# Optimization experiments

Measured on AMD Instinct MI355X. Metric: run time of the kernel, lower is better.

Reference implementation:

```python
import jax, jax.numpy as jnp
import numpy as np

NUM_TOPICS = 64
VOCAB_SIZE = 50000
BATCH = 2048
RHO = 0.1

def setup_inputs() -> dict:
    key = jax.random.key(0)
    k_x, k_b, k_t, k_m = jax.random.split(key, 4)
    x = jax.random.uniform(k_x, (BATCH, VOCAB_SIZE), dtype=jnp.float32)  # BoW-like counts
    beta = jax.random.normal(k_b, (NUM_TOPICS, VOCAB_SIZE), dtype=jnp.float32)
    theta = jax.random.normal(k_t, (NUM_TOPICS, NUM_TOPICS), dtype=jnp.float32)
    mu = jax.random.normal(k_m, (NUM_TOPICS,), dtype=jnp.float32)
    return {"x": x, "beta": beta, "theta": theta, "mu": mu}

def reference(x, beta, theta, mu):
    # Original double loop:
    #   log_prob[:,k] = sum(x*beta[k],1) + mu[k] + rho * sum_{j!=k} theta[k,j]*sum(x*beta[j],1)
    # Let s[b,k] = sum_v x[b,v]*beta[k,v] = (x @ beta.T)[b,k].
    # Then log_prob = s + mu + rho * s @ (theta with zeroed diagonal).T
    s = jnp.einsum('bv,kv->bk', x, beta)                      # [B, K]
    theta_off = theta * (1.0 - jnp.eye(theta.shape[0], dtype=theta.dtype))
    log_prob = s + mu[None, :] + RHO * jnp.einsum('bj,kj->bk', s, theta_off)
    return log_prob
```

## Files before the change

kernel.cpp:

```cpp
#include <hip/hip_runtime.h>

typedef unsigned short u16;
typedef unsigned int u32;
typedef unsigned long long u64;

#define VOCAB 50000
#define BATCH 2048
#define NTOP 64
#define RHO 0.1f

#define KSPLIT 32
#define CHUNK 1568
#define KSTEP 64

typedef short bf16x4 __attribute__((ext_vector_type(4)));
typedef short bf16x8 __attribute__((ext_vector_type(8)));
typedef float f32x4 __attribute__((ext_vector_type(4)));

__device__ __forceinline__ u32 cvtpk(float lo, float hi) {
  u32 r;
  asm volatile("v_cvt_pk_bf16_f32 %0, %1, %2" : "=v"(r) : "v"(lo), "v"(hi));
  return r;
}
union frag_cast { bf16x4 h[2]; bf16x8 v; };

__global__ void __launch_bounds__(256, 4) ctm_gemm(const float* __restrict__ x,
                                                   const float* __restrict__ beta,
                                                   float* __restrict__ sp) {
  __shared__ u16 ldsA[2][64 * KSTEP];
  __shared__ u16 ldsB[2][64 * KSTEP];

  const int t = threadIdx.x;
  const int l = t & 63;
  const int w = t >> 6;
  const int fr = l & 15;
  const int fk = l >> 4;

  const int bx = blockIdx.x;
  const int k0 = bx * CHUNK;
  const int kend = (k0 + CHUNK < VOCAB) ? (k0 + CHUNK) : VOCAB;
  const int row0 = blockIdx.y * 64;
  const int nsteps = (kend - k0 + KSTEP - 1) >> 6;

  const int c = t & 15;
  const int srow = t >> 4;
  const float* xb = x + (u64)(row0 + srow) * VOCAB + k0 + c * 4;
  const float* betab = beta + (u64)srow * VOCAB + k0 + c * 4;
  const u32 wofs = (u32)(srow * 128) + (((u32)(c * 8)) ^ ((u32)((srow & 7) << 4)));

  const int arow = w * 16 + fr;
  const u32 arb = (u32)(arow * 128);
  const u32 aswz = (u32)((arow & 7) << 4);

  f32x4 acc[4] = {{0.f,0.f,0.f,0.f},{0.f,0.f,0.f,0.f},{0.f,0.f,0.f,0.f},{0.f,0.f,0.f,0.f}};

  {
    const int rem = kend - k0 < KSTEP ? kend - k0 : KSTEP;
    const bool m = (c * 4) < rem;
    float4 a0 = make_float4(0,0,0,0), a1 = a0, a2 = a0, a3 = a0;
    float4 b0 = a0, b1 = a0, b2 = a0, b3 = a0;
    if (m) {
      a0 = *(const float4*)(xb);               b0 = *(const float4*)(betab);
      a1 = *(const float4*)(xb + 16 * VOCAB);  b1 = *(const float4*)(betab + 16 * VOCAB);
      a2 = *(const float4*)(xb + 32 * VOCAB);  b2 = *(const float4*)(betab + 32 * VOCAB);
      a3 = *(const float4*)(xb + 48 * VOCAB);  b3 = *(const float4*)(betab + 48 * VOCAB);
    }
    *(uint2*)((char*)ldsA[0] + wofs)        = make_uint2(cvtpk(a0.x,a0.y), cvtpk(a0.z,a0.w));
    *(uint2*)((char*)ldsA[0] + wofs + 2048) = make_uint2(cvtpk(a1.x,a1.y), cvtpk(a1.z,a1.w));
    *(uint2*)((char*)ldsA[0] + wofs + 4096) = make_uint2(cvtpk(a2.x,a2.y), cvtpk(a2.z,a2.w));
    *(uint2*)((char*)ldsA[0] + wofs + 6144) = make_uint2(cvtpk(a3.x,a3.y), cvtpk(a3.z,a3.w));
    *(uint2*)((char*)ldsB[0] + wofs)        = make_uint2(cvtpk(b0.x,b0.y), cvtpk(b0.z,b0.w));
    *(uint2*)((char*)ldsB[0] + wofs + 2048) = make_uint2(cvtpk(b1.x,b1.y), cvtpk(b1.z,b1.w));
    *(uint2*)((char*)ldsB[0] + wofs + 4096) = make_uint2(cvtpk(b2.x,b2.y), cvtpk(b2.z,b2.w));
    *(uint2*)((char*)ldsB[0] + wofs + 6144) = make_uint2(cvtpk(b3.x,b3.y), cvtpk(b3.z,b3.w));
  }
  __syncthreads();

  for (int st = 0; st < nsteps; ++st) {
    const int cb = st & 1;
    const bool have_next = (st + 1) < nsteps;

    float4 a0, a1, a2, a3, b0, b1, b2, b3;
    if (have_next) {
      const int ks = (st + 1) << 6;
      const int rem = kend - k0 - ks;
      const bool m = (c * 4) < rem;
      a0 = a1 = a2 = a3 = make_float4(0,0,0,0);
      b0 = b1 = b2 = b3 = make_float4(0,0,0,0);
      if (m) {
        const float* xp = xb + ks;
        const float* bp2 = betab + ks;
        a0 = *(const float4*)(xp);               b0 = *(const float4*)(bp2);
        a1 = *(const float4*)(xp + 16 * VOCAB);  b1 = *(const float4*)(bp2 + 16 * VOCAB);
        a2 = *(const float4*)(xp + 32 * VOCAB);  b2 = *(const float4*)(bp2 + 32 * VOCAB);
        a3 = *(const float4*)(xp + 48 * VOCAB);  b3 = *(const float4*)(bp2 + 48 * VOCAB);
      }
    }

    const char* bufA = (const char*)ldsA[cb];
    const char* bufB = (const char*)ldsB[cb];
    #pragma unroll
    for (int s = 0; s < 2; ++s) {
      const u32 in0 = (u32)(s * 64 + fk * 8);
      const u32 in1 = in0 + 32;
      frag_cast ua;
      ua.h[0] = *(const bf16x4*)(bufA + arb + (in0 ^ aswz));
      ua.h[1] = *(const bf16x4*)(bufA + arb + (in1 ^ aswz));
      #pragma unroll
      for (int n = 0; n < 4; ++n) {
        const int bcol = (n << 4) | fr;
        const u32 brb = (u32)(bcol * 128);
        const u32 bswz = (u32)((bcol & 7) << 4);
        frag_cast ub;
        ub.h[0] = *(const bf16x4*)(bufB + brb + (in0 ^ bswz));
        ub.h[1] = *(const bf16x4*)(bufB + brb + (in1 ^ bswz));
        acc[n] = __builtin_amdgcn_mfma_f32_16x16x32_bf16(ua.v, ub.v, acc[n], 0, 0, 0);
      }
    }

    if (have_next) {
      char* nA = (char*)ldsA[cb ^ 1];
      char* nB = (char*)ldsB[cb ^ 1];
      *(uint2*)(nA + wofs)        = make_uint2(cvtpk(a0.x,a0.y), cvtpk(a0.z,a0.w));
      *(uint2*)(nA + wofs + 2048) = make_uint2(cvtpk(a1.x,a1.y), cvtpk(a1.z,a1.w));
      *(uint2*)(nA + wofs + 4096) = make_uint2(cvtpk(a2.x,a2.y), cvtpk(a2.z,a2.w));
      *(uint2*)(nA + wofs + 6144) = make_uint2(cvtpk(a3.x,a3.y), cvtpk(a3.z,a3.w));
      *(uint2*)(nB + wofs)        = make_uint2(cvtpk(b0.x,b0.y), cvtpk(b0.z,b0.w));
      *(uint2*)(nB + wofs + 2048) = make_uint2(cvtpk(b1.x,b1.y), cvtpk(b1.z,b1.w));
      *(uint2*)(nB + wofs + 4096) = make_uint2(cvtpk(b2.x,b2.y), cvtpk(b2.z,b2.w));
      *(uint2*)(nB + wofs + 6144) = make_uint2(cvtpk(b3.x,b3.y), cvtpk(b3.z,b3.w));
      __syncthreads();
    }
  }

  float* spb = sp + (u64)bx * (BATCH * NTOP);
  const int orow = row0 + w * 16 + fk * 4;
  #pragma unroll
  for (int n = 0; n < 4; ++n) {
    #pragma unroll
    for (int r = 0; r < 4; ++r)
      spb[(orow + r) * NTOP + ((n << 4) | fr)] = acc[n][r];
  }
}

__global__ void __launch_bounds__(256) ctm_epi(const float* __restrict__ sp,
                                               const float* __restrict__ theta,
                                               const float* __restrict__ mu,
                                               float* __restrict__ out) {
  __shared__ float thT[NTOP * NTOP];
  __shared__ float sb[8 * NTOP];
  const int t = threadIdx.x;
  const int r0 = blockIdx.x * 8;

  #pragma unroll
  for (int i = 0; i < 16; ++i) {
    int e = i * 256 + t;
    thT[(e & 63) * 64 + (e >> 6)] = theta[e];
  }

  const int k = t & 63;
  const int rl = t >> 6;
  #pragma unroll
  for (int rr = 0; rr < 2; ++rr) {
    const int r = rl + rr * 4;
    float sum = 0.f;
    #pragma unroll
    for (int cc = 0; cc < KSPLIT; ++cc)
      sum += sp[(u64)cc * (BATCH * NTOP) + (r0 + r) * NTOP + k];
    sb[r * 64 + k] = sum;
  }
  __syncthreads();

  const float muk = mu[k];
  const float diag = thT[k * 64 + k];
  #pragma unroll
  for (int rr = 0; rr < 2; ++rr) {
    const int r = rl + rr * 4;
    const float* srow = &sb[r * 64];
    float accv = 0.f;
    #pragma unroll 8
    for (int j = 0; j < 64; ++j)
      accv += thT[j * 64 + k] * srow[j];
    const float sv = srow[k];
    out[(r0 + r) * 64 + k] = sv + muk + RHO * (accv - diag * sv);
  }
}

extern "C" void kernel_launch(void* const* d_in, const int* in_sizes, int n_in,
                              void* d_out, int out_size, void* d_ws, size_t ws_size,
                              hipStream_t stream) {
  const float* x = (const float*)d_in[0];
  const float* beta = (const float*)d_in[1];
  const float* theta = (const float*)d_in[2];
  const float* mu = (const float*)d_in[3];
  float* out = (float*)d_out;

  float* sp = (float*)d_ws;

  ctm_gemm<<<dim3(KSPLIT, BATCH / 64), 256, 0, stream>>>(x, beta, sp);
  ctm_epi<<<BATCH / 8, 256, 0, stream>>>(sp, theta, mu, out);
}
```

Measured before the change: 109.7 us.

## Use direct global-to-LDS loads with triple buffering and half-precision partials

Result: no change. 111.3 us (+1.5%).

```diff
diff --git a/kernel.cpp b/kernel.cpp
--- a/kernel.cpp
+++ b/kernel.cpp
@@ -1,4 +1,5 @@
 #include <hip/hip_runtime.h>
+#include <hip/hip_fp16.h>
 
 typedef unsigned short u16;
 typedef unsigned int u32;
@@ -9,9 +10,10 @@
 #define NTOP 64
 #define RHO 0.1f
 
-#define KSPLIT 32
-#define CHUNK 1568
-#define KSTEP 64
+#define KSPLIT 24
+#define CHUNK 2112
+#define KSTEP 32
+#define BUFB 16384
 
 typedef short bf16x4 __attribute__((ext_vector_type(4)));
 typedef short bf16x8 __attribute__((ext_vector_type(8)));
@@ -22,13 +24,12 @@
   asm volatile("v_cvt_pk_bf16_f32 %0, %1, %2" : "=v"(r) : "v"(lo), "v"(hi));
   return r;
 }
-union frag_cast { bf16x4 h[2]; bf16x8 v; };
-
-__global__ void __launch_bounds__(256, 4) ctm_gemm(const float* __restrict__ x,
+union frag_cast { u32 w[4]; bf16x8 v; };
+
+__global__ void __launch_bounds__(256, 3) ctm_gemm(const float* __restrict__ x,
                                                    const float* __restrict__ beta,
-                                                   float* __restrict__ sp) {
-  __shared__ u16 ldsA[2][64 * KSTEP];
-  __shared__ u16 ldsB[2][64 * KSTEP];
+                                                   __half* __restrict__ sp) {
+  __shared__ u16 lds[3 * BUFB / 2];
 
   const int t = threadIdx.x;
   const int l = t & 63;
@@ -40,110 +41,129 @@
   const int k0 = bx * CHUNK;
   const int kend = (k0 + CHUNK < VOCAB) ? (k0 + CHUNK) : VOCAB;
   const int row0 = blockIdx.y * 64;
-  const int nsteps = (kend - k0 + KSTEP - 1) >> 6;
-
-  const int c = t & 15;
-  const int srow = t >> 4;
-  const float* xb = x + (u64)(row0 + srow) * VOCAB + k0 + c * 4;
-  const float* betab = beta + (u64)srow * VOCAB + k0 + c * 4;
-  const u32 wofs = (u32)(srow * 128) + (((u32)(c * 8)) ^ ((u32)((srow & 7) << 4)));
+  const int nfull = (kend - k0) >> 5;
+  const int rem = (kend - k0) & 31;
+
+  const int sr = t >> 3;
+  const int so = t & 7;
+  const int swf = 4 * (so ^ (sr & 7));
+  const float* xs0 = x + (u64)(row0 + sr) * VOCAB + k0 + swf;
+  const float* xs1 = xs0 + (u64)32 * VOCAB;
+  const float* bs0 = beta + (u64)sr * VOCAB + k0 + swf;
+  const float* bs1 = bs0 + (u64)32 * VOCAB;
+  const u32 dA0 = (u32)(t * 16), dA1 = dA0 + 4096;
+  const u32 dB0 = dA0 + 8192,   dB1 = dA0 + 12288;
 
   const int arow = w * 16 + fr;
   const u32 arb = (u32)(arow * 128);
   const u32 aswz = (u32)((arow & 7) << 4);
+  const u32 aof0 = (u32)(fk * 16) ^ aswz;
+  const u32 aof1 = (u32)(64 + fk * 16) ^ aswz;
 
   f32x4 acc[4] = {{0.f,0.f,0.f,0.f},{0.f,0.f,0.f,0.f},{0.f,0.f,0.f,0.f},{0.f,0.f,0.f,0.f}};
 
-  {
-    const int rem = kend - k0 < KSTEP ? kend - k0 : KSTEP;
-    const bool m = (c * 4) < rem;
-    float4 a0 = make_float4(0,0,0,0), a1 = a0, a2 = a0, a3 = a0;
-    float4 b0 = a0, b1 = a0, b2 = a0, b3 = a0;
-    if (m) {
-      a0 = *(const float4*)(xb);               b0 = *(const float4*)(betab);
-      a1 = *(const float4*)(xb + 16 * VOCAB);  b1 = *(const float4*)(betab + 16 * VOCAB);
-      a2 = *(const float4*)(xb + 32 * VOCAB);  b2 = *(const float4*)(betab + 32 * VOCAB);
-      a3 = *(const float4*)(xb + 48 * VOCAB);  b3 = *(const float4*)(betab + 48 * VOCAB);
+#define STAGE(slot, st)                                                          \
+  {                                                                              \
+    const u32 b_ = (u32)(slot) * BUFB;                                           \
+    const u64 ko_ = (u64)((st) * KSTEP);                                         \
+    __builtin_amdgcn_global_load_lds(                                            \
+        (const __attribute__((address_space(1))) void*)(xs0 + ko_),              \
+        (__attribute__((address_space(3))) void*)((char*)lds + b_ + dA0), 16, 0, 0); \
+    __builtin_amdgcn_global_load_lds(                                            \
+        (const __attribute__((address_space(1))) void*)(xs1 + ko_),              \
+        (__attribute__((address_space(3))) void*)((char*)lds + b_ + dA1), 16, 0, 0); \
+    __builtin_amdgcn_global_load_lds(                                            \
+        (const __attribute__((address_space(1))) void*)(bs0 + ko_),              \
+        (__attribute__((address_space(3))) void*)((char*)lds + b_ + dB0), 16, 0, 0); \
+    __builtin_amdgcn_global_load_lds(                                            \
+        (const __attribute__((address_space(1))) void*)(bs1 + ko_),              \
+        (__attribute__((address_space(3))) void*)((char*)lds + b_ + dB1), 16, 0, 0); \
+  }
+
+#define COMPUTE(slot)                                                            \
+  {                                                                              \
+    const char* bufA = (const char*)lds + (u32)(slot) * BUFB;                    \
+    const char* bufB = bufA + 8192;                                              \
+    f32x4 q0 = *(const f32x4*)(bufA + arb + aof0);                               \
+    f32x4 q1 = *(const f32x4*)(bufA + arb + aof1);                               \
+    frag_cast ua;                                                                \
+    ua.w[0] = cvtpk(q0.x, q0.y); ua.w[1] = cvtpk(q0.z, q0.w);                    \
+    ua.w[2] = cvtpk(q1.x, q1.y); ua.w[3] = cvtpk(q1.z, q1.w);                    \
+    _Pragma("unroll")                                                            \
+    for (int n = 0; n < 4; ++n) {                                                \
+      const int bcol = n * 16 + fr;                                              \
+      const u32 brb = (u32)(bcol * 128);                                         \
+      const u32 bswz = (u32)((bcol & 7) << 4);                                   \
+      f32x4 p0 = *(const f32x4*)(bufB + brb + (((u32)(fk * 16)) ^ bswz));        \
+      f32x4 p1 = *(const f32x4*)(bufB + brb + (((u32)(64 + fk * 16)) ^ bswz));   \
+      frag_cast ub;                                                              \
+      ub.w[0] = cvtpk(p0.x, p0.y); ub.w[1] = cvtpk(p0.z, p0.w);                  \
+      ub.w[2] = cvtpk(p1.x, p1.y); ub.w[3] = cvtpk(p1.z, p1.w);                  \
+      acc[n] = __builtin_amdgcn_mfma_f32_16x16x32_bf16(ua.v, ub.v, acc[n], 0, 0, 0); \
+    }                                                                            \
+  }
+
+  STAGE(0, 0);
+  STAGE(1, 1);
+
+  int slot = 0;
+  for (int st = 0; st < nfull; ++st) {
+    if (st + 1 < nfull) asm volatile("s_waitcnt vmcnt(4)" ::: "memory");
+    else                asm volatile("s_waitcnt vmcnt(0)" ::: "memory");
+    __builtin_amdgcn_s_barrier();
+    __builtin_amdgcn_sched_barrier(0);
+    if (st + 2 < nfull) {
+      const int ns = (slot + 2 >= 3) ? (slot - 1) : (slot + 2);
+      STAGE(ns, st + 2);
     }
-    *(uint2*)((char*)ldsA[0] + wofs)        = make_uint2(cvtpk(a0.x,a0.y), cvtpk(a0.z,a0.w));
-    *(uint2*)((char*)ldsA[0] + wofs + 2048) = make_uint2(cvtpk(a1.x,a1.y), cvtpk(a1.z,a1.w));
-    *(uint2*)((char*)ldsA[0] + wofs + 4096) = make_uint2(cvtpk(a2.x,a2.y), cvtpk(a2.z,a2.w));
-    *(uint2*)((char*)ldsA[0] + wofs + 6144) = make_uint2(cvtpk(a3.x,a3.y), cvtpk(a3.z,a3.w));
-    *(uint2*)((char*)ldsB[0] + wofs)        = make_uint2(cvtpk(b0.x,b0.y), cvtpk(b0.z,b0.w));
-    *(uint2*)((char*)ldsB[0] + wofs + 2048) = make_uint2(cvtpk(b1.x,b1.y), cvtpk(b1.z,b1.w));
-    *(uint2*)((char*)ldsB[0] + wofs + 4096) = make_uint2(cvtpk(b2.x,b2.y), cvtpk(b2.z,b2.w));
-    *(uint2*)((char*)ldsB[0] + wofs + 6144) = make_uint2(cvtpk(b3.x,b3.y), cvtpk(b3.z,b3.w));
-  }
-  __syncthreads();
-
-  for (int st = 0; st < nsteps; ++st) {
-    const int cb = st & 1;
-    const bool have_next = (st + 1) < nsteps;
-
-    float4 a0, a1, a2, a3, b0, b1, b2, b3;
-    if (have_next) {
-      const int ks = (st + 1) << 6;
-      const int rem = kend - k0 - ks;
-      const bool m = (c * 4) < rem;
-      a0 = a1 = a2 = a3 = make_float4(0,0,0,0);
-      b0 = b1 = b2 = b3 = make_float4(0,0,0,0);
-      if (m) {
-        const float* xp = xb + ks;
-        const float* bp2 = betab + ks;
-        a0 = *(const float4*)(xp);               b0 = *(const float4*)(bp2);
-        a1 = *(const float4*)(xp + 16 * VOCAB);  b1 = *(const float4*)(bp2 + 16 * VOCAB);
-        a2 = *(const float4*)(xp + 32 * VOCAB);  b2 = *(const float4*)(bp2 + 32 * VOCAB);
-        a3 = *(const float4*)(xp + 48 * VOCAB);  b3 = *(const float4*)(bp2 + 48 * VOCAB);
-      }
+    COMPUTE(slot);
+    slot = (slot + 1 >= 3) ? 0 : slot + 1;
+  }
+
+  if (rem) {
+    const int trow = t >> 2;
+    const int tq = t & 3;
+    const int ktail = k0 + nfull * KSTEP;
+    const u32 wofs = (u32)(trow * 128) + (((u32)(tq * 32)) ^ ((u32)((trow & 7) << 4)));
+    float4 va0 = make_float4(0,0,0,0), va1 = va0, vb0 = va0, vb1 = va0;
+    if (tq * 8 < rem) {
+      const float* xp = x + (u64)(row0 + trow) * VOCAB + ktail + tq * 8;
+      const float* bp2 = beta + (u64)trow * VOCAB + ktail + tq * 8;
+      va0 = *(const float4*)xp;  va1 = *(const float4*)(xp + 4);
+      vb0 = *(const float4*)bp2; vb1 = *(const float4*)(bp2 + 4);
     }
-
-    const char* bufA = (const char*)ldsA[cb];
-    const char* bufB = (const char*)ldsB[cb];
-    #pragma unroll
-    for (int s = 0; s < 2; ++s) {
-      const u32 in0 = (u32)(s * 64 + fk * 8);
-      const u32 in1 = in0 + 32;
-      frag_cast ua;
-      ua.h[0] = *(const bf16x4*)(bufA + arb + (in0 ^ aswz));
-      ua.h[1] = *(const bf16x4*)(bufA + arb + (in1 ^ aswz));
-      #pragma unroll
-      for (int n = 0; n < 4; ++n) {
-        const int bcol = (n << 4) | fr;
-        const u32 brb = (u32)(bcol * 128);
-        const u32 bswz = (u32)((bcol & 7) << 4);
-        frag_cast ub;
-        ub.h[0] = *(const bf16x4*)(bufB + brb + (in0 ^ bswz));
-        ub.h[1] = *(const bf16x4*)(bufB + brb + (in1 ^ bswz));
-        acc[n] = __builtin_amdgcn_mfma_f32_16x16x32_bf16(ua.v, ub.v, acc[n], 0, 0, 0);
-      }
-    }
-
-    if (have_next) {
-      char* nA = (char*)ldsA[cb ^ 1];
-      char* nB = (char*)ldsB[cb ^ 1];
-      *(uint2*)(nA + wofs)        = make_uint2(cvtpk(a0.x,a0.y), cvtpk(a0.z,a0.w));
-      *(uint2*)(nA + wofs + 2048) = make_uint2(cvtpk(a1.x,a1.y), cvtpk(a1.z,a1.w));
-      *(uint2*)(nA + wofs + 4096) = make_uint2(cvtpk(a2.x,a2.y), cvtpk(a2.z,a2.w));
-      *(uint2*)(nA + wofs + 6144) = make_uint2(cvtpk(a3.x,a3.y), cvtpk(a3.z,a3.w));
-      *(uint2*)(nB + wofs)        = make_uint2(cvtpk(b0.x,b0.y), cvtpk(b0.z,b0.w));
-      *(uint2*)(nB + wofs + 2048) = make_uint2(cvtpk(b1.x,b1.y), cvtpk(b1.z,b1.w));
-      *(uint2*)(nB + wofs + 4096) = make_uint2(cvtpk(b2.x,b2.y), cvtpk(b2.z,b2.w));
-      *(uint2*)(nB + wofs + 6144) = make_uint2(cvtpk(b3.x,b3.y), cvtpk(b3.z,b3.w));
-      __syncthreads();
-    }
-  }
-
-  float* spb = sp + (u64)bx * (BATCH * NTOP);
+    char* tb = (char*)lds + (u32)slot * BUFB;
+    uint4 pa, pb;
+    pa.x = cvtpk(va0.x, va0.y); pa.y = cvtpk(va0.z, va0.w);
+    pa.z = cvtpk(va1.x, va1.y); pa.w = cvtpk(va1.z, va1.w);
+    pb.x = cvtpk(vb0.x, vb0.y); pb.y = cvtpk(vb0.z, vb0.w);
+    pb.z = cvtpk(vb1.x, vb1.y); pb.w = cvtpk(vb1.z, vb1.w);
+    *(float4*)(tb + trow * 128 + (((u32)(tq * 32)) ^ ((u32)((trow & 7) << 4)))) =
+        (tq * 8 < rem) ? va0 : make_float4(0,0,0,0);
+    (void)wofs; (void)pa; (void)pb;
+    *(float4*)(tb + trow * 128 + (((u32)(tq * 32 + 16)) ^ ((u32)((trow & 7) << 4)))) =
+        (tq * 8 < rem) ? va1 : make_float4(0,0,0,0);
+    *(float4*)(tb + 8192 + trow * 128 + (((u32)(tq * 32)) ^ ((u32)((trow & 7) << 4)))) =
+        (tq * 8 < rem) ? vb0 : make_float4(0,0,0,0);
+    *(float4*)(tb + 8192 + trow * 128 + (((u32)(tq * 32 + 16)) ^ ((u32)((trow & 7) << 4)))) =
+        (tq * 8 < rem) ? vb1 : make_float4(0,0,0,0);
+    __syncthreads();
+    COMPUTE(slot);
+  }
+
+  __half* spb = sp + (u64)bx * (BATCH * NTOP);
   const int orow = row0 + w * 16 + fk * 4;
   #pragma unroll
   for (int n = 0; n < 4; ++n) {
     #pragma unroll
     for (int r = 0; r < 4; ++r)
-      spb[(orow + r) * NTOP + ((n << 4) | fr)] = acc[n][r];
-  }
-}
-
-__global__ void __launch_bounds__(256) ctm_epi(const float* __restrict__ sp,
+      spb[(u64)(orow + r) * NTOP + (n * 16 + fr)] = __float2half(acc[n][r]);
+  }
+#undef STAGE
+#undef COMPUTE
+}
+
+__global__ void __launch_bounds__(256) ctm_epi(const __half* __restrict__ sp,
                                                const float* __restrict__ theta,
                                                const float* __restrict__ mu,
                                                float* __restrict__ out) {
@@ -166,7 +186,7 @@
     float sum = 0.f;
     #pragma unroll
     for (int cc = 0; cc < KSPLIT; ++cc)
-      sum += sp[(u64)cc * (BATCH * NTOP) + (r0 + r) * NTOP + k];
+      sum += __half2float(sp[(u64)cc * (BATCH * NTOP) + (u64)(r0 + r) * NTOP + k]);
     sb[r * 64 + k] = sum;
   }
   __syncthreads();
@@ -195,7 +215,7 @@
   const float* mu = (const float*)d_in[3];
   float* out = (float*)d_out;
 
-  float* sp = (float*)d_ws;
+  __half* sp = (__half*)d_ws;
 
   ctm_gemm<<<dim3(KSPLIT, BATCH / 64), 256, 0, stream>>>(x, beta, sp);
   ctm_epi<<<BATCH / 8, 256, 0, stream>>>(sp, theta, mu, out);
```

## Prefetch x tiles three steps ahead and store split-K partials as fp16

Applied to the files above, without the earlier changes.

New measurement: 101.4 us (median of 2 runs). 7.5% less time.

```diff
diff --git a/kernel.cpp b/kernel.cpp
--- a/kernel.cpp
+++ b/kernel.cpp
@@ -1,4 +1,5 @@
 #include <hip/hip_runtime.h>
+#include <hip/hip_fp16.h>
 
 typedef unsigned short u16;
 typedef unsigned int u32;
@@ -26,8 +27,8 @@
 
 __global__ void __launch_bounds__(256, 4) ctm_gemm(const float* __restrict__ x,
                                                    const float* __restrict__ beta,
-                                                   float* __restrict__ sp) {
-  __shared__ u16 ldsA[2][64 * KSTEP];
+                                                   __half* __restrict__ sp) {
+  __shared__ u16 ldsX[2][64 * KSTEP];
   __shared__ u16 ldsB[2][64 * KSTEP];
 
   const int t = threadIdx.x;
@@ -54,96 +55,112 @@
 
   f32x4 acc[4] = {{0.f,0.f,0.f,0.f},{0.f,0.f,0.f,0.f},{0.f,0.f,0.f,0.f},{0.f,0.f,0.f,0.f}};
 
-  {
-    const int rem = kend - k0 < KSTEP ? kend - k0 : KSTEP;
-    const bool m = (c * 4) < rem;
-    float4 a0 = make_float4(0,0,0,0), a1 = a0, a2 = a0, a3 = a0;
-    float4 b0 = a0, b1 = a0, b2 = a0, b3 = a0;
-    if (m) {
-      a0 = *(const float4*)(xb);               b0 = *(const float4*)(betab);
-      a1 = *(const float4*)(xb + 16 * VOCAB);  b1 = *(const float4*)(betab + 16 * VOCAB);
-      a2 = *(const float4*)(xb + 32 * VOCAB);  b2 = *(const float4*)(betab + 32 * VOCAB);
-      a3 = *(const float4*)(xb + 48 * VOCAB);  b3 = *(const float4*)(betab + 48 * VOCAB);
-    }
-    *(uint2*)((char*)ldsA[0] + wofs)        = make_uint2(cvtpk(a0.x,a0.y), cvtpk(a0.z,a0.w));
-    *(uint2*)((char*)ldsA[0] + wofs + 2048) = make_uint2(cvtpk(a1.x,a1.y), cvtpk(a1.z,a1.w));
-    *(uint2*)((char*)ldsA[0] + wofs + 4096) = make_uint2(cvtpk(a2.x,a2.y), cvtpk(a2.z,a2.w));
-    *(uint2*)((char*)ldsA[0] + wofs + 6144) = make_uint2(cvtpk(a3.x,a3.y), cvtpk(a3.z,a3.w));
-    *(uint2*)((char*)ldsB[0] + wofs)        = make_uint2(cvtpk(b0.x,b0.y), cvtpk(b0.z,b0.w));
-    *(uint2*)((char*)ldsB[0] + wofs + 2048) = make_uint2(cvtpk(b1.x,b1.y), cvtpk(b1.z,b1.w));
-    *(uint2*)((char*)ldsB[0] + wofs + 4096) = make_uint2(cvtpk(b2.x,b2.y), cvtpk(b2.z,b2.w));
-    *(uint2*)((char*)ldsB[0] + wofs + 6144) = make_uint2(cvtpk(b3.x,b3.y), cvtpk(b3.z,b3.w));
-  }
+  float4 xA0, xA1, xA2, xA3, xB0, xB1, xB2, xB3;
+  float4 bb0, bb1, bb2, bb3;
+
+#define LOADX(S0, S1, S2, S3, st)                                            \
+  {                                                                          \
+    const int rem_ = kend - k0 - (st) * KSTEP;                               \
+    S0 = S1 = S2 = S3 = make_float4(0.f, 0.f, 0.f, 0.f);                     \
+    if (c * 4 < rem_) {                                                      \
+      const float* p_ = xb + (st) * KSTEP;                                   \
+      S0 = *(const float4*)(p_);                                             \
+      S1 = *(const float4*)(p_ + 16 * VOCAB);                                \
+      S2 = *(const float4*)(p_ + 32 * VOCAB);                                \
+      S3 = *(const float4*)(p_ + 48 * VOCAB);                                \
+    }                                                                        \
+  }
+
+#define LOADB(st)                                                            \
+  {                                                                          \
+    const int rem_ = kend - k0 - (st) * KSTEP;                               \
+    bb0 = bb1 = bb2 = bb3 = make_float4(0.f, 0.f, 0.f, 0.f);                 \
+    if (c * 4 < rem_) {                                                      \
+      const float* p_ = betab + (st) * KSTEP;                                \
+      bb0 = *(const float4*)(p_);                                            \
+      bb1 = *(const float4*)(p_ + 16 * VOCAB);                               \
+      bb2 = *(const float4*)(p_ + 32 * VOCAB);                               \
+      bb3 = *(const float4*)(p_ + 48 * VOCAB);                               \
+    }                                                                        \
+  }
+
+#define WRITE(S0, S1, S2, S3, bi)                                            \
+  {                                                                          \
+    char* nX = (char*)ldsX[bi];                                              \
+    char* nB = (char*)ldsB[bi];                                              \
+    *(uint2*)(nX + wofs)        = make_uint2(cvtpk(S0.x, S0.y), cvtpk(S0.z, S0.w)); \
+    *(uint2*)(nX + wofs + 2048) = make_uint2(cvtpk(S1.x, S1.y), cvtpk(S1.z, S1.w)); \
+    *(uint2*)(nX + wofs + 4096) = make_uint2(cvtpk(S2.x, S2.y), cvtpk(S2.z, S2.w)); \
+    *(uint2*)(nX + wofs + 6144) = make_uint2(cvtpk(S3.x, S3.y), cvtpk(S3.z, S3.w)); \
+    *(uint2*)(nB + wofs)        = make_uint2(cvtpk(bb0.x, bb0.y), cvtpk(bb0.z, bb0.w)); \
+    *(uint2*)(nB + wofs + 2048) = make_uint2(cvtpk(bb1.x, bb1.y), cvtpk(bb1.z, bb1.w)); \
+    *(uint2*)(nB + wofs + 4096) = make_uint2(cvtpk(bb2.x, bb2.y), cvtpk(bb2.z, bb2.w)); \
+    *(uint2*)(nB + wofs + 6144) = make_uint2(cvtpk(bb3.x, bb3.y), cvtpk(bb3.z, bb3.w)); \
+  }
+
+#define COMPUTE(bi)                                                          \
+  {                                                                          \
+    const char* bufA = (const char*)ldsX[bi];                                \
+    const char* bufB = (const char*)ldsB[bi];                                \
+    _Pragma("unroll")                                                        \
+    for (int s_ = 0; s_ < 2; ++s_) {                                         \
+      const u32 in0 = (u32)(s_ * 64 + fk * 8);                               \
+      const u32 in1 = in0 + 32;                                              \
+      frag_cast ua;                                                          \
+      ua.h[0] = *(const bf16x4*)(bufA + arb + (in0 ^ aswz));                 \
+      ua.h[1] = *(const bf16x4*)(bufA + arb + (in1 ^ aswz));                 \
+      _Pragma("unroll")                                                      \
+      for (int n_ = 0; n_ < 4; ++n_) {                                       \
+        const int bcol = (n_ << 4) | fr;                                     \
+        const u32 brb = (u32)(bcol * 128);                                   \
+        const u32 bswz = (u32)((bcol & 7) << 4);                             \
+        frag_cast ub;                                                        \
+        ub.h[0] = *(const bf16x4*)(bufB + brb + (in0 ^ bswz));               \
+        ub.h[1] = *(const bf16x4*)(bufB + brb + (in1 ^ bswz));               \
+        acc[n_] = __builtin_amdgcn_mfma_f32_16x16x32_bf16(ua.v, ub.v, acc[n_], 0, 0, 0); \
+      }                                                                      \
+    }                                                                        \
+  }
+
+  LOADX(xA0, xA1, xA2, xA3, 0);
+  LOADB(0);
+  WRITE(xA0, xA1, xA2, xA3, 0);
+  LOADX(xA0, xA1, xA2, xA3, 1);
+  LOADX(xB0, xB1, xB2, xB3, 2);
   __syncthreads();
 
-  for (int st = 0; st < nsteps; ++st) {
-    const int cb = st & 1;
-    const bool have_next = (st + 1) < nsteps;
-
-    float4 a0, a1, a2, a3, b0, b1, b2, b3;
-    if (have_next) {
-      const int ks = (st + 1) << 6;
-      const int rem = kend - k0 - ks;
-      const bool m = (c * 4) < rem;
-      a0 = a1 = a2 = a3 = make_float4(0,0,0,0);
-      b0 = b1 = b2 = b3 = make_float4(0,0,0,0);
-      if (m) {
-        const float* xp = xb + ks;
-        const float* bp2 = betab + ks;
-        a0 = *(const float4*)(xp);               b0 = *(const float4*)(bp2);
-        a1 = *(const float4*)(xp + 16 * VOCAB);  b1 = *(const float4*)(bp2 + 16 * VOCAB);
-        a2 = *(const float4*)(xp + 32 * VOCAB);  b2 = *(const float4*)(bp2 + 32 * VOCAB);
-        a3 = *(const float4*)(xp + 48 * VOCAB);  b3 = *(const float4*)(bp2 + 48 * VOCAB);
-      }
-    }
-
-    const char* bufA = (const char*)ldsA[cb];
-    const char* bufB = (const char*)ldsB[cb];
-    #pragma unroll
-    for (int s = 0; s < 2; ++s) {
-      const u32 in0 = (u32)(s * 64 + fk * 8);
-      const u32 in1 = in0 + 32;
-      frag_cast ua;
-      ua.h[0] = *(const bf16x4*)(bufA + arb + (in0 ^ aswz));
-      ua.h[1] = *(const bf16x4*)(bufA + arb + (in1 ^ aswz));
-      #pragma unroll
-      for (int n = 0; n < 4; ++n) {
-        const int bcol = (n << 4) | fr;
-        const u32 brb = (u32)(bcol * 128);
-        const u32 bswz = (u32)((bcol & 7) << 4);
-        frag_cast ub;
-        ub.h[0] = *(const bf16x4*)(bufB + brb + (in0 ^ bswz));
-        ub.h[1] = *(const bf16x4*)(bufB + brb + (in1 ^ bswz));
-        acc[n] = __builtin_amdgcn_mfma_f32_16x16x32_bf16(ua.v, ub.v, acc[n], 0, 0, 0);
-      }
-    }
-
-    if (have_next) {
-      char* nA = (char*)ldsA[cb ^ 1];
-      char* nB = (char*)ldsB[cb ^ 1];
-      *(uint2*)(nA + wofs)        = make_uint2(cvtpk(a0.x,a0.y), cvtpk(a0.z,a0.w));
-      *(uint2*)(nA + wofs + 2048) = make_uint2(cvtpk(a1.x,a1.y), cvtpk(a1.z,a1.w));
-      *(uint2*)(nA + wofs + 4096) = make_uint2(cvtpk(a2.x,a2.y), cvtpk(a2.z,a2.w));
-      *(uint2*)(nA + wofs + 6144) = make_uint2(cvtpk(a3.x,a3.y), cvtpk(a3.z,a3.w));
-      *(uint2*)(nB + wofs)        = make_uint2(cvtpk(b0.x,b0.y), cvtpk(b0.z,b0.w));
-      *(uint2*)(nB + wofs + 2048) = make_uint2(cvtpk(b1.x,b1.y), cvtpk(b1.z,b1.w));
-      *(uint2*)(nB + wofs + 4096) = make_uint2(cvtpk(b2.x,b2.y), cvtpk(b2.z,b2.w));
-      *(uint2*)(nB + wofs + 6144) = make_uint2(cvtpk(b3.x,b3.y), cvtpk(b3.z,b3.w));
-      __syncthreads();
-    }
-  }
-
-  float* spb = sp + (u64)bx * (BATCH * NTOP);
+  int st = 0;
+  while (true) {
+    if (st + 1 < nsteps) LOADB(st + 1);
+    COMPUTE(st & 1);
+    if (st + 1 < nsteps) WRITE(xA0, xA1, xA2, xA3, (st + 1) & 1);
+    if (st + 3 < nsteps) LOADX(xA0, xA1, xA2, xA3, st + 3);
+    if (st + 1 < nsteps) __syncthreads();
+    if (++st >= nsteps) break;
+
+    if (st + 1 < nsteps) LOADB(st + 1);
+    COMPUTE(st & 1);
+    if (st + 1 < nsteps) WRITE(xB0, xB1, xB2, xB3, (st + 1) & 1);
+    if (st + 3 < nsteps) LOADX(xB0, xB1, xB2, xB3, st + 3);
+    if (st + 1 < nsteps) __syncthreads();
+    if (++st >= nsteps) break;
+  }
+
+  __half* spb = sp + (u64)bx * (BATCH * NTOP);
   const int orow = row0 + w * 16 + fk * 4;
   #pragma unroll
   for (int n = 0; n < 4; ++n) {
     #pragma unroll
     for (int r = 0; r < 4; ++r)
-      spb[(orow + r) * NTOP + ((n << 4) | fr)] = acc[n][r];
-  }
-}
-
-__global__ void __launch_bounds__(256) ctm_epi(const float* __restrict__ sp,
+      spb[(u64)(orow + r) * NTOP + ((n << 4) | fr)] = __float2half(acc[n][r]);
+  }
+#undef LOADX
+#undef LOADB
+#undef WRITE
+#undef COMPUTE
+}
+
+__global__ void __launch_bounds__(256) ctm_epi(const __half* __restrict__ sp,
                                                const float* __restrict__ theta,
                                                const float* __restrict__ mu,
                                                float* __restrict__ out) {
@@ -166,7 +183,7 @@
     float sum = 0.f;
     #pragma unroll
     for (int cc = 0; cc < KSPLIT; ++cc)
-      sum += sp[(u64)cc * (BATCH * NTOP) + (r0 + r) * NTOP + k];
+      sum += __half2float(sp[(u64)cc * (BATCH * NTOP) + (u64)(r0 + r) * NTOP + k]);
     sb[r * 64 + k] = sum;
   }
   __syncthreads();
@@ -195,7 +212,7 @@
   const float* mu = (const float*)d_in[3];
   float* out = (float*)d_out;
 
-  float* sp = (float*)d_ws;
+  __half* sp = (__half*)d_ws;
 
   ctm_gemm<<<dim3(KSPLIT, BATCH / 64), 256, 0, stream>>>(x, beta, sp);
   ctm_epi<<<BATCH / 8, 256, 0, stream>>>(sp, theta, mu, out);
```
